# Optimization experiments

Hardware: AMD Instinct MI355X
Metric: run time of the kernel (lower is better)

The kernel has to match this reference:

```python
import jax, jax.numpy as jnp
import numpy as np

D_MODEL = 1024
NUM_HEADS = 8
D_K = D_MODEL // NUM_HEADS


def setup_inputs() -> dict:
    key = jax.random.key(0)
    ks = jax.random.split(key, 11)
    B, S, D = 2, 2048, D_MODEL
    scale = 1.0 / np.sqrt(D)
    return {
        "Q": jax.random.normal(ks[0], (B, S, D), jnp.float32),
        "K": jax.random.normal(ks[1], (B, S, D), jnp.float32),
        "V": jax.random.normal(ks[2], (B, S, D), jnp.float32),
        # torch nn.Linear weights are stored (out_features, in_features)
        "Wq": jax.random.normal(ks[3], (D, D), jnp.float32) * scale,
        "bq": jnp.zeros((D,), jnp.float32),
        "Wk": jax.random.normal(ks[4], (D, D), jnp.float32) * scale,
        "bk": jnp.zeros((D,), jnp.float32),
        "Wv": jax.random.normal(ks[5], (D, D), jnp.float32) * scale,
        "bv": jnp.zeros((D,), jnp.float32),
        "Wo": jax.random.normal(ks[6], (D, D), jnp.float32) * scale,
        "bo": jnp.zeros((D,), jnp.float32),
    }


def reference(Q, K, V, Wq, bq, Wk, bk, Wv, bv, Wo, bo):
    B, S, D = Q.shape
    H, dk = NUM_HEADS, D_K
    # projections (torch Linear: x @ W.T + b), then split heads -> [B,H,S,dk]
    q = (Q @ Wq.T + bq).reshape(B, S, H, dk).transpose(0, 2, 1, 3)
    k = (K @ Wk.T + bk).reshape(B, S, H, dk).transpose(0, 2, 1, 3)
    v = (V @ Wv.T + bv).reshape(B, S, H, dk).transpose(0, 2, 1, 3)
    scores = jnp.einsum("bhqd,bhkd->bhqk", q, k) / jnp.sqrt(jnp.float32(dk))
    attn = jax.nn.softmax(scores, axis=-1)  # [B,H,S,S]
    ctx = jnp.einsum("bhqk,bhkd->bhqd", attn, v)
    concat = ctx.transpose(0, 2, 1, 3).reshape(B, S, D)
    out = concat @ Wo.T + bo
    return out, attn
```

## Files before the change

### kernel.cpp

```cpp
#include <hip/hip_runtime.h>

#define S_LEN 2048
#define DMODEL 1024
#define NHEADS 8
#define DK 128
#define BATCH 2

typedef _Float16 h16;
typedef __attribute__((ext_vector_type(8))) _Float16 half8v;
typedef __attribute__((ext_vector_type(4))) float float4v;

#define GLD16(gp, lp)                                                  \
  __builtin_amdgcn_global_load_lds(                                    \
      (const __attribute__((address_space(1))) void*)(gp),             \
      (__attribute__((address_space(3))) void*)(lp), 16, 0, 0)

__global__ __launch_bounds__(256) void cvt_all(
    const float* __restrict__ q, const float* __restrict__ k, const float* __restrict__ v,
    const float* __restrict__ wq, const float* __restrict__ wk, const float* __restrict__ wv,
    const float* __restrict__ wo,
    h16* __restrict__ dq, h16* __restrict__ dk, h16* __restrict__ dv,
    h16* __restrict__ dwq, h16* __restrict__ dwk, h16* __restrict__ dwv,
    h16* __restrict__ dwo) {
  int i = blockIdx.x * 256 + threadIdx.x;
  const float* src;
  h16* dst;
  int off;
  if (i < 1572864) {
    int seg = i >> 19;
    off = i & 524287;
    src = seg == 0 ? q : (seg == 1 ? k : v);
    dst = seg == 0 ? dq : (seg == 1 ? dk : dv);
  } else {
    int j = i - 1572864;
    int seg = j >> 17;
    off = j & 131071;
    src = seg == 0 ? wq : (seg == 1 ? wk : (seg == 2 ? wv : wo));
    dst = seg == 0 ? dwq : (seg == 1 ? dwk : (seg == 2 ? dwv : dwo));
  }
  const float4* s = (const float4*)src + (size_t)off * 2;
  float4 a = s[0], b = s[1];
  half8v h = {(h16)a.x, (h16)a.y, (h16)a.z, (h16)a.w,
              (h16)b.x, (h16)b.y, (h16)b.z, (h16)b.w};
  *((half8v*)dst + off) = h;
}

__global__ __launch_bounds__(256) void qkv_gemm(
    const h16* __restrict__ qf, const h16* __restrict__ kf, const h16* __restrict__ vf,
    const h16* __restrict__ wq, const h16* __restrict__ wk, const h16* __restrict__ wv,
    const float* __restrict__ bq, const float* __restrict__ bk, const float* __restrict__ bv,
    h16* __restrict__ qh, h16* __restrict__ kh, h16* __restrict__ vt) {
  __shared__ h16 As[128 * 32];
  __shared__ h16 Bs[128 * 32];

  const int z = blockIdx.z;
  const h16* A = z == 0 ? qf : (z == 1 ? kf : vf);
  const h16* Bw = z == 0 ? wq : (z == 1 ? wk : wv);
  const float* bias = z == 0 ? bq : (z == 1 ? bk : bv);
  h16* outp = z == 0 ? qh : (z == 1 ? kh : vt);

  const int t = threadIdx.x, lane = t & 63, w = t >> 6;
  const int m0 = blockIdx.y * 128, n0 = blockIdx.x * 128;
  const int wm = (w >> 1) * 64, wn = (w & 1) * 64;
  const int lcol = lane & 15, lquad = lane >> 4;

  float4v acc[4][4];
  for (int i = 0; i < 4; ++i)
    for (int j = 0; j < 4; ++j) acc[i][j] = {0.f, 0.f, 0.f, 0.f};

  for (int kt = 0; kt < 1024; kt += 32) {
    __syncthreads();
    for (int j = 0; j < 2; ++j) {
      int i = w * 2 + j;
      int row = i * 16 + (lane >> 2);
      int c4 = (lane & 3) ^ ((row >> 1) & 3);
      GLD16(A + (size_t)(m0 + row) * 1024 + kt + c4 * 8, As + i * 512);
      GLD16(Bw + (size_t)(n0 + row) * 1024 + kt + c4 * 8, Bs + i * 512);
    }
    __syncthreads();

    half8v af[4], bf[4];
    for (int mi = 0; mi < 4; ++mi) {
      int r = wm + mi * 16 + lcol;
      af[mi] = *(const half8v*)(As + r * 32 + ((lquad ^ ((r >> 1) & 3)) << 3));
    }
    for (int ni = 0; ni < 4; ++ni) {
      int r = wn + ni * 16 + lcol;
      bf[ni] = *(const half8v*)(Bs + r * 32 + ((lquad ^ ((r >> 1) & 3)) << 3));
    }
    for (int mi = 0; mi < 4; ++mi)
      for (int ni = 0; ni < 4; ++ni)
        acc[mi][ni] = __builtin_amdgcn_mfma_f32_16x16x32_f16(af[mi], bf[ni],
                                                             acc[mi][ni], 0, 0, 0);
  }

  for (int ni = 0; ni < 4; ++ni) {
    int gn = n0 + wn + ni * 16 + lcol;
    float bvv = bias[gn];
    int hh = gn >> 7, dv = gn & 127;
    for (int mi = 0; mi < 4; ++mi) {
      int gmb = m0 + wm + mi * 16 + lquad * 4;
      for (int r = 0; r < 4; ++r) {
        int gm = gmb + r;
        float v = acc[mi][ni][r] + bvv;
        int b = gm >> 11, s = gm & 2047;
        if (z < 2)
          outp[((size_t)(b * NHEADS + hh) * S_LEN + s) * DK + dv] = (h16)v;
        else
          outp[((size_t)(b * NHEADS + hh) * DK + dv) * S_LEN + s] = (h16)v;
      }
    }
  }
}

__global__ __launch_bounds__(256) void out_gemm(const h16* __restrict__ A,
                                                const h16* __restrict__ Bw,
                                                const float* __restrict__ bias,
                                                float* __restrict__ C) {
  __shared__ h16 As[64 * 32];
  __shared__ h16 Bs[128 * 32];

  const int t = threadIdx.x, lane = t & 63, w = t >> 6;
  const int m0 = blockIdx.y * 64, n0 = blockIdx.x * 128;
  const int wm = (w >> 1) * 32, wn = (w & 1) * 64;
  const int lcol = lane & 15, lquad = lane >> 4;

  float4v acc[2][4];
  for (int i = 0; i < 2; ++i)
    for (int j = 0; j < 4; ++j) acc[i][j] = {0.f, 0.f, 0.f, 0.f};

  for (int kt = 0; kt < 1024; kt += 32) {
    __syncthreads();
    {
      int i = w;
      int row = i * 16 + (lane >> 2);
      int c4 = (lane & 3) ^ ((row >> 1) & 3);
      GLD16(A + (size_t)(m0 + row) * 1024 + kt + c4 * 8, As + i * 512);
    }
    for (int j = 0; j < 2; ++j) {
      int i = w * 2 + j;
      int row = i * 16 + (lane >> 2);
      int c4 = (lane & 3) ^ ((row >> 1) & 3);
      GLD16(Bw + (size_t)(n0 + row) * 1024 + kt + c4 * 8, Bs + i * 512);
    }
    __syncthreads();

    half8v af[2], bf[4];
    for (int mi = 0; mi < 2; ++mi) {
      int r = wm + mi * 16 + lcol;
      af[mi] = *(const half8v*)(As + r * 32 + ((lquad ^ ((r >> 1) & 3)) << 3));
    }
    for (int ni = 0; ni < 4; ++ni) {
      int r = wn + ni * 16 + lcol;
      bf[ni] = *(const half8v*)(Bs + r * 32 + ((lquad ^ ((r >> 1) & 3)) << 3));
    }
    for (int mi = 0; mi < 2; ++mi)
      for (int ni = 0; ni < 4; ++ni)
        acc[mi][ni] = __builtin_amdgcn_mfma_f32_16x16x32_f16(af[mi], bf[ni],
                                                             acc[mi][ni], 0, 0, 0);
  }

  for (int ni = 0; ni < 4; ++ni) {
    int gn = n0 + wn + ni * 16 + lcol;
    float bvv = bias[gn];
    for (int mi = 0; mi < 2; ++mi) {
      int gmb = m0 + wm + mi * 16 + lquad * 4;
      for (int r = 0; r < 4; ++r)
        C[(size_t)(gmb + r) * 1024 + gn] = acc[mi][ni][r] + bvv;
    }
  }
}

__device__ inline void attn_bid(int& bh, int& q0) {
  int id = blockIdx.y * 32 + blockIdx.x;
  int xcd = id & 7, rank = id >> 3;
  bh = xcd + 8 * (rank >> 5);
  q0 = (rank & 31) * 64;
}

#define PV_STEP(PP, VV)                                                        \
  {                                                                            \
    half8v ap[4][2];                                                           \
    for (int mi = 0; mi < 4; ++mi)                                             \
      for (int k2 = 0; k2 < 2; ++k2)                                           \
        ap[mi][k2] =                                                           \
            *(const half8v*)((PP) + (mi * 16 + lcol) * 72 + k2 * 32 + lquad * 8); \
    for (int nd = 0; nd < 2; ++nd) {                                           \
      int r = w * 32 + nd * 16 + lcol;                                         \
      for (int k2 = 0; k2 < 2; ++k2) {                                         \
        half8v bv = *(const half8v*)((VV) + r * 64 +                           \
                                     (((k2 * 4 + lquad) ^ (r & 7)) << 3));     \
        for (int mi = 0; mi < 4; ++mi)                                         \
          cacc[mi][nd] = __builtin_amdgcn_mfma_f32_16x16x32_f16(               \
              ap[mi][k2], bv, cacc[mi][nd], 0, 0, 0);                          \
      }                                                                        \
    }                                                                          \
  }

__global__ __launch_bounds__(256, 2) void attn_fused(
    const h16* __restrict__ qh, const h16* __restrict__ kh,
    const h16* __restrict__ vt, float* __restrict__ attn,
    h16* __restrict__ ctxb) {
  __shared__ h16 Ks[64 * 128];
  __shared__ h16 Vts[2][128 * 64];
  __shared__ h16 Ps[2][64 * 72];

  const int t = threadIdx.x, lane = t & 63, w = t >> 6;
  const int lcol = lane & 15, lquad = lane >> 4;
  int bh, q0;
  attn_bid(bh, q0);
  const int b = bh >> 3, h = bh & 7;
  const float scale = 0.08838834764831845f;

  for (int j = 0; j < 4; ++j) {
    int i = w * 4 + j;
    int row = i * 4 + (lane >> 4);
    int c4 = (lane & 15) ^ (row & 7);
    GLD16(qh + ((size_t)bh * S_LEN + q0 + row) * DK + c4 * 8, Ks + i * 512);
  }
  __syncthreads();
  half8v aq[4][4];
  for (int mi = 0; mi < 4; ++mi) {
    int r = mi * 16 + lcol;
    for (int ks = 0; ks < 4; ++ks)
      aq[mi][ks] = *(const half8v*)(Ks + r * 128 + (((ks * 4 + lquad) ^ (r & 7)) << 3));
  }

  float ls[4][4];
  for (int mi = 0; mi < 4; ++mi)
    for (int rr = 0; rr < 4; ++rr) ls[mi][rr] = 0.f;

  for (int kt = 0; kt < 32; ++kt) {
    __syncthreads();
    for (int j = 0; j < 4; ++j) {
      int i = w * 4 + j;
      int row = i * 4 + (lane >> 4);
      int c4 = (lane & 15) ^ (row & 7);
      GLD16(kh + ((size_t)bh * S_LEN + kt * 64 + row) * DK + c4 * 8, Ks + i * 512);
    }
    __syncthreads();

    float4v sacc[4];
    for (int mi = 0; mi < 4; ++mi) sacc[mi] = {0.f, 0.f, 0.f, 0.f};
    int r = w * 16 + lcol;
    for (int ks = 0; ks < 4; ++ks) {
      half8v bk = *(const half8v*)(Ks + r * 128 + (((ks * 4 + lquad) ^ (r & 7)) << 3));
      for (int mi = 0; mi < 4; ++mi)
        sacc[mi] = __builtin_amdgcn_mfma_f32_16x16x32_f16(aq[mi][ks], bk, sacc[mi], 0, 0, 0);
    }
    for (int mi = 0; mi < 4; ++mi)
      for (int rr = 0; rr < 4; ++rr) ls[mi][rr] += __expf(sacc[mi][rr] * scale);
  }

  float* red = (float*)Ps[0];
  for (int mi = 0; mi < 4; ++mi)
    for (int rr = 0; rr < 4; ++rr) {
      float vsum = ls[mi][rr];
      for (int off = 1; off < 16; off <<= 1) vsum += __shfl_xor(vsum, off);
      if (lcol == 0) red[w * 64 + mi * 16 + lquad * 4 + rr] = vsum;
    }
  __syncthreads();
  float il[4][4];
  for (int mi = 0; mi < 4; ++mi)
    for (int rr = 0; rr < 4; ++rr) {
      int row = mi * 16 + lquad * 4 + rr;
      il[mi][rr] = 1.f / (red[row] + red[64 + row] + red[128 + row] + red[192 + row]);
    }

  float4v cacc[4][2];
  for (int mi = 0; mi < 4; ++mi)
    for (int nd = 0; nd < 2; ++nd) cacc[mi][nd] = {0.f, 0.f, 0.f, 0.f};

  float* abase = attn + ((size_t)bh * S_LEN + q0 + lquad * 4) * S_LEN + w * 16 + lcol;

  for (int kt = 0; kt < 32; ++kt) {
    int p = kt & 1;
    __syncthreads();
    for (int j = 0; j < 4; ++j) {
      int i = w * 4 + j;
      int row = i * 4 + (lane >> 4);
      int c4 = (lane & 15) ^ (row & 7);
      GLD16(kh + ((size_t)bh * S_LEN + kt * 64 + row) * DK + c4 * 8, Ks + i * 512);
    }
    for (int j = 0; j < 4; ++j) {
      int i = w * 4 + j;
      int row = i * 8 + (lane >> 3);
      int c4 = (lane & 7) ^ (row & 7);
      GLD16(vt + ((size_t)bh * DK + row) * S_LEN + kt * 64 + c4 * 8, Vts[p] + i * 512);
    }
    __syncthreads();

    if (kt > 0) {
      const h16* Psr = Ps[p ^ 1];
      const h16* Vr = Vts[p ^ 1];
      PV_STEP(Psr, Vr);
    }

    float4v sacc[4];
    for (int mi = 0; mi < 4; ++mi) sacc[mi] = {0.f, 0.f, 0.f, 0.f};
    {
      int r = w * 16 + lcol;
      for (int ks = 0; ks < 4; ++ks) {
        half8v bk = *(const half8v*)(Ks + r * 128 + (((ks * 4 + lquad) ^ (r & 7)) << 3));
        for (int mi = 0; mi < 4; ++mi)
          sacc[mi] = __builtin_amdgcn_mfma_f32_16x16x32_f16(aq[mi][ks], bk, sacc[mi], 0, 0, 0);
      }
    }

    h16* Psw = Ps[p] + lquad * 4 * 72 + w * 16 + lcol;
    float* ab = abase + (size_t)kt * 64;
    for (int mi = 0; mi < 4; ++mi)
      for (int rr = 0; rr < 4; ++rr) {
        float pv = __expf(sacc[mi][rr] * scale) * il[mi][rr];
        ab[(size_t)(mi * 16 + rr) * S_LEN] = pv;
        Psw[(mi * 16 + rr) * 72] = (h16)pv;
      }
  }

  __syncthreads();
  {
    const h16* Psr = Ps[1];
    const h16* Vr = Vts[1];
    PV_STEP(Psr, Vr);
  }

  h16* cb = ctxb + ((size_t)b * S_LEN + q0 + lquad * 4) * DMODEL + h * DK + w * 32;
  for (int mi = 0; mi < 4; ++mi)
    for (int nd = 0; nd < 2; ++nd)
      for (int rr = 0; rr < 4; ++rr)
        cb[(size_t)(mi * 16 + rr) * DMODEL + nd * 16 + lcol] = (h16)cacc[mi][nd][rr];
}

extern "C" void kernel_launch(void* const* d_in, const int* in_sizes, int n_in,
                              void* d_out, int out_size, void* d_ws, size_t ws_size,
                              hipStream_t stream) {
  const float* Q  = (const float*)d_in[0];
  const float* K  = (const float*)d_in[1];
  const float* V  = (const float*)d_in[2];
  const float* Wq = (const float*)d_in[3];
  const float* bq = (const float*)d_in[4];
  const float* Wk = (const float*)d_in[5];
  const float* bk = (const float*)d_in[6];
  const float* Wv = (const float*)d_in[7];
  const float* bv = (const float*)d_in[8];
  const float* Wo = (const float*)d_in[9];
  const float* bo = (const float*)d_in[10];

  float* out  = (float*)d_out;
  float* attn = out + (size_t)BATCH * S_LEN * DMODEL;

  const size_t NTOK = (size_t)BATCH * S_LEN * DMODEL;
  const size_t NW = (size_t)DMODEL * DMODEL;
  h16* qf  = (h16*)d_ws;
  h16* kf  = qf + NTOK;
  h16* vf  = kf + NTOK;
  h16* wqh = vf + NTOK;
  h16* wkh = wqh + NW;
  h16* wvh = wkh + NW;
  h16* woh = wvh + NW;
  h16* qh  = woh + NW;
  h16* kh  = qh + NTOK;
  h16* vt  = kh + NTOK;
  h16* ctxb = qf;

  dim3 gb(256);
  cvt_all<<<dim3(8192), gb, 0, stream>>>(Q, K, V, Wq, Wk, Wv, Wo,
                                         qf, kf, vf, wqh, wkh, wvh, woh);
  qkv_gemm<<<dim3(8, 32, 3), gb, 0, stream>>>(qf, kf, vf, wqh, wkh, wvh,
                                              bq, bk, bv, qh, kh, vt);
  attn_fused<<<dim3(32, 16), gb, 0, stream>>>(qh, kh, vt, attn, ctxb);
  out_gemm<<<dim3(8, 64), gb, 0, stream>>>(ctxb, woh, bo, out);
}
```

Baseline: 471.7 us.

## Double-buffer LDS tiles with explicit waitcnt barriers in GEMMs and attention

The QKV and output GEMMs now use ping-pong LDS buffers. The next K-tile is prefetched through global_load_lds while MFMAs run on the current one, and each iteration ends with a single s_waitcnt+s_barrier instead of two __syncthreads. The attention kernel also double-buffers its K tiles in both passes. Its PV product moves into the same iteration as the score computation with a single P buffer, and a partial vmcnt(16) wait is meant to avoid draining the attention-probability stores each step. The gain should come from overlapping memory latency with compute. The cost is more LDS per block, and the hand-written vmcnt counting relies on the ordering of in-flight loads and stores.

```diff
diff --git a/kernel.cpp b/kernel.cpp
--- a/kernel.cpp
+++ b/kernel.cpp
@@ -14,6 +14,22 @@
   __builtin_amdgcn_global_load_lds(                                    \
       (const __attribute__((address_space(1))) void*)(gp),             \
       (__attribute__((address_space(3))) void*)(lp), 16, 0, 0)
+
+#define BAR_VM0()                                                       \
+  do {                                                                  \
+    asm volatile("s_waitcnt vmcnt(0) lgkmcnt(0)\ns_barrier" ::: "memory"); \
+    __builtin_amdgcn_sched_barrier(0);                                  \
+  } while (0)
+#define BAR_VM16()                                                      \
+  do {                                                                  \
+    asm volatile("s_waitcnt vmcnt(16) lgkmcnt(0)\ns_barrier" ::: "memory"); \
+    __builtin_amdgcn_sched_barrier(0);                                  \
+  } while (0)
+#define BAR_LGKM()                                                      \
+  do {                                                                  \
+    asm volatile("s_waitcnt lgkmcnt(0)\ns_barrier" ::: "memory");       \
+    __builtin_amdgcn_sched_barrier(0);                                  \
+  } while (0)
 
 __global__ __launch_bounds__(256) void cvt_all(
     const float* __restrict__ q, const float* __restrict__ k, const float* __restrict__ v,
@@ -50,8 +66,8 @@
     const h16* __restrict__ wq, const h16* __restrict__ wk, const h16* __restrict__ wv,
     const float* __restrict__ bq, const float* __restrict__ bk, const float* __restrict__ bv,
     h16* __restrict__ qh, h16* __restrict__ kh, h16* __restrict__ vt) {
-  __shared__ h16 As[128 * 32];
-  __shared__ h16 Bs[128 * 32];
+  __shared__ h16 As[2][128 * 32];
+  __shared__ h16 Bs[2][128 * 32];
 
   const int z = blockIdx.z;
   const h16* A = z == 0 ? qf : (z == 1 ? kf : vf);
@@ -68,30 +84,38 @@
   for (int i = 0; i < 4; ++i)
     for (int j = 0; j < 4; ++j) acc[i][j] = {0.f, 0.f, 0.f, 0.f};
 
-  for (int kt = 0; kt < 1024; kt += 32) {
-    __syncthreads();
-    for (int j = 0; j < 2; ++j) {
-      int i = w * 2 + j;
-      int row = i * 16 + (lane >> 2);
-      int c4 = (lane & 3) ^ ((row >> 1) & 3);
-      GLD16(A + (size_t)(m0 + row) * 1024 + kt + c4 * 8, As + i * 512);
-      GLD16(Bw + (size_t)(n0 + row) * 1024 + kt + c4 * 8, Bs + i * 512);
-    }
-    __syncthreads();
-
+#define QKV_STAGE(S, P)                                                    \
+  for (int j = 0; j < 2; ++j) {                                            \
+    int i = w * 2 + j;                                                     \
+    int row = i * 16 + (lane >> 2);                                        \
+    int c4 = (lane & 3) ^ ((row >> 1) & 3);                                \
+    GLD16(A + (size_t)(m0 + row) * 1024 + (S) * 32 + c4 * 8, As[P] + i * 512); \
+    GLD16(Bw + (size_t)(n0 + row) * 1024 + (S) * 32 + c4 * 8, Bs[P] + i * 512); \
+  }
+
+  QKV_STAGE(0, 0);
+  BAR_VM0();
+
+  for (int s = 0; s < 32; ++s) {
+    int sn = s + 1 < 32 ? s + 1 : s;
+    QKV_STAGE(sn, (s + 1) & 1);
+
+    const h16* Ar = As[s & 1];
+    const h16* Br = Bs[s & 1];
     half8v af[4], bf[4];
     for (int mi = 0; mi < 4; ++mi) {
       int r = wm + mi * 16 + lcol;
-      af[mi] = *(const half8v*)(As + r * 32 + ((lquad ^ ((r >> 1) & 3)) << 3));
+      af[mi] = *(const half8v*)(Ar + r * 32 + ((lquad ^ ((r >> 1) & 3)) << 3));
     }
     for (int ni = 0; ni < 4; ++ni) {
       int r = wn + ni * 16 + lcol;
-      bf[ni] = *(const half8v*)(Bs + r * 32 + ((lquad ^ ((r >> 1) & 3)) << 3));
+      bf[ni] = *(const half8v*)(Br + r * 32 + ((lquad ^ ((r >> 1) & 3)) << 3));
     }
     for (int mi = 0; mi < 4; ++mi)
       for (int ni = 0; ni < 4; ++ni)
         acc[mi][ni] = __builtin_amdgcn_mfma_f32_16x16x32_f16(af[mi], bf[ni],
                                                              acc[mi][ni], 0, 0, 0);
+    BAR_VM0();
   }
 
   for (int ni = 0; ni < 4; ++ni) {
@@ -103,11 +127,11 @@
       for (int r = 0; r < 4; ++r) {
         int gm = gmb + r;
         float v = acc[mi][ni][r] + bvv;
-        int b = gm >> 11, s = gm & 2047;
+        int b = gm >> 11, sdx = gm & 2047;
         if (z < 2)
-          outp[((size_t)(b * NHEADS + hh) * S_LEN + s) * DK + dv] = (h16)v;
+          outp[((size_t)(b * NHEADS + hh) * S_LEN + sdx) * DK + dv] = (h16)v;
         else
-          outp[((size_t)(b * NHEADS + hh) * DK + dv) * S_LEN + s] = (h16)v;
+          outp[((size_t)(b * NHEADS + hh) * DK + dv) * S_LEN + sdx] = (h16)v;
       }
     }
   }
@@ -117,8 +141,8 @@
                                                 const h16* __restrict__ Bw,
                                                 const float* __restrict__ bias,
                                                 float* __restrict__ C) {
-  __shared__ h16 As[64 * 32];
-  __shared__ h16 Bs[128 * 32];
+  __shared__ h16 As[2][64 * 32];
+  __shared__ h16 Bs[2][128 * 32];
 
   const int t = threadIdx.x, lane = t & 63, w = t >> 6;
   const int m0 = blockIdx.y * 64, n0 = blockIdx.x * 128;
@@ -129,35 +153,42 @@
   for (int i = 0; i < 2; ++i)
     for (int j = 0; j < 4; ++j) acc[i][j] = {0.f, 0.f, 0.f, 0.f};
 
-  for (int kt = 0; kt < 1024; kt += 32) {
-    __syncthreads();
-    {
-      int i = w;
-      int row = i * 16 + (lane >> 2);
-      int c4 = (lane & 3) ^ ((row >> 1) & 3);
-      GLD16(A + (size_t)(m0 + row) * 1024 + kt + c4 * 8, As + i * 512);
-    }
-    for (int j = 0; j < 2; ++j) {
-      int i = w * 2 + j;
-      int row = i * 16 + (lane >> 2);
-      int c4 = (lane & 3) ^ ((row >> 1) & 3);
-      GLD16(Bw + (size_t)(n0 + row) * 1024 + kt + c4 * 8, Bs + i * 512);
-    }
-    __syncthreads();
-
+#define OUT_STAGE(S, P)                                                    \
+  {                                                                        \
+    int row = w * 16 + (lane >> 2);                                        \
+    int c4 = (lane & 3) ^ ((row >> 1) & 3);                                \
+    GLD16(A + (size_t)(m0 + row) * 1024 + (S) * 32 + c4 * 8, As[P] + w * 512); \
+    for (int j = 0; j < 2; ++j) {                                          \
+      int i = w * 2 + j;                                                   \
+      int row2 = i * 16 + (lane >> 2);                                     \
+      int c42 = (lane & 3) ^ ((row2 >> 1) & 3);                            \
+      GLD16(Bw + (size_t)(n0 + row2) * 1024 + (S) * 32 + c42 * 8, Bs[P] + i * 512); \
+    }                                                                      \
+  }
+
+  OUT_STAGE(0, 0);
+  BAR_VM0();
+
+  for (int s = 0; s < 32; ++s) {
+    int sn = s + 1 < 32 ? s + 1 : s;
+    OUT_STAGE(sn, (s + 1) & 1);
+
+    const h16* Ar = As[s & 1];
+    const h16* Br = Bs[s & 1];
     half8v af[2], bf[4];
     for (int mi = 0; mi < 2; ++mi) {
       int r = wm + mi * 16 + lcol;
-      af[mi] = *(const half8v*)(As + r * 32 + ((lquad ^ ((r >> 1) & 3)) << 3));
+      af[mi] = *(const half8v*)(Ar + r * 32 + ((lquad ^ ((r >> 1) & 3)) << 3));
     }
     for (int ni = 0; ni < 4; ++ni) {
       int r = wn + ni * 16 + lcol;
-      bf[ni] = *(const half8v*)(Bs + r * 32 + ((lquad ^ ((r >> 1) & 3)) << 3));
+      bf[ni] = *(const half8v*)(Br + r * 32 + ((lquad ^ ((r >> 1) & 3)) << 3));
     }
     for (int mi = 0; mi < 2; ++mi)
       for (int ni = 0; ni < 4; ++ni)
         acc[mi][ni] = __builtin_amdgcn_mfma_f32_16x16x32_f16(af[mi], bf[ni],
                                                              acc[mi][ni], 0, 0, 0);
+    BAR_VM0();
   }
 
   for (int ni = 0; ni < 4; ++ni) {
@@ -178,32 +209,13 @@
   q0 = (rank & 31) * 64;
 }
 
-#define PV_STEP(PP, VV)                                                        \
-  {                                                                            \
-    half8v ap[4][2];                                                           \
-    for (int mi = 0; mi < 4; ++mi)                                             \
-      for (int k2 = 0; k2 < 2; ++k2)                                           \
-        ap[mi][k2] =                                                           \
-            *(const half8v*)((PP) + (mi * 16 + lcol) * 72 + k2 * 32 + lquad * 8); \
-    for (int nd = 0; nd < 2; ++nd) {                                           \
-      int r = w * 32 + nd * 16 + lcol;                                         \
-      for (int k2 = 0; k2 < 2; ++k2) {                                         \
-        half8v bv = *(const half8v*)((VV) + r * 64 +                           \
-                                     (((k2 * 4 + lquad) ^ (r & 7)) << 3));     \
-        for (int mi = 0; mi < 4; ++mi)                                         \
-          cacc[mi][nd] = __builtin_amdgcn_mfma_f32_16x16x32_f16(               \
-              ap[mi][k2], bv, cacc[mi][nd], 0, 0, 0);                          \
-      }                                                                        \
-    }                                                                          \
-  }
-
 __global__ __launch_bounds__(256, 2) void attn_fused(
     const h16* __restrict__ qh, const h16* __restrict__ kh,
     const h16* __restrict__ vt, float* __restrict__ attn,
     h16* __restrict__ ctxb) {
-  __shared__ h16 Ks[64 * 128];
+  __shared__ h16 Ks[2][64 * 128];
   __shared__ h16 Vts[2][128 * 64];
-  __shared__ h16 Ps[2][64 * 72];
+  __shared__ h16 Ps[64 * 72];
 
   const int t = threadIdx.x, lane = t & 63, w = t >> 6;
   const int lcol = lane & 15, lquad = lane >> 4;
@@ -212,47 +224,62 @@
   const int b = bh >> 3, h = bh & 7;
   const float scale = 0.08838834764831845f;
 
+#define STAGE_K(KT, BUF)                                                     \
+  for (int j = 0; j < 4; ++j) {                                              \
+    int i = w * 4 + j;                                                       \
+    int row = i * 4 + (lane >> 4);                                           \
+    int c4 = (lane & 15) ^ (row & 7);                                        \
+    GLD16(kh + ((size_t)bh * S_LEN + (KT) * 64 + row) * DK + c4 * 8,         \
+          (BUF) + i * 512);                                                  \
+  }
+#define STAGE_V(KT, BUF)                                                     \
+  for (int j = 0; j < 4; ++j) {                                              \
+    int i = w * 4 + j;                                                       \
+    int row = i * 8 + (lane >> 3);                                           \
+    int c4 = (lane & 7) ^ (row & 7);                                         \
+    GLD16(vt + ((size_t)bh * DK + row) * S_LEN + (KT) * 64 + c4 * 8,         \
+          (BUF) + i * 512);                                                  \
+  }
+
   for (int j = 0; j < 4; ++j) {
     int i = w * 4 + j;
     int row = i * 4 + (lane >> 4);
     int c4 = (lane & 15) ^ (row & 7);
-    GLD16(qh + ((size_t)bh * S_LEN + q0 + row) * DK + c4 * 8, Ks + i * 512);
-  }
-  __syncthreads();
+    GLD16(qh + ((size_t)bh * S_LEN + q0 + row) * DK + c4 * 8, Ks[0] + i * 512);
+  }
+  BAR_VM0();
+  STAGE_K(0, Ks[1]);
   half8v aq[4][4];
   for (int mi = 0; mi < 4; ++mi) {
     int r = mi * 16 + lcol;
     for (int ks = 0; ks < 4; ++ks)
-      aq[mi][ks] = *(const half8v*)(Ks + r * 128 + (((ks * 4 + lquad) ^ (r & 7)) << 3));
-  }
+      aq[mi][ks] = *(const half8v*)(Ks[0] + r * 128 + (((ks * 4 + lquad) ^ (r & 7)) << 3));
+  }
+  BAR_VM0();
 
   float ls[4][4];
   for (int mi = 0; mi < 4; ++mi)
     for (int rr = 0; rr < 4; ++rr) ls[mi][rr] = 0.f;
 
-  for (int kt = 0; kt < 32; ++kt) {
-    __syncthreads();
-    for (int j = 0; j < 4; ++j) {
-      int i = w * 4 + j;
-      int row = i * 4 + (lane >> 4);
-      int c4 = (lane & 15) ^ (row & 7);
-      GLD16(kh + ((size_t)bh * S_LEN + kt * 64 + row) * DK + c4 * 8, Ks + i * 512);
-    }
-    __syncthreads();
-
+  for (int s = 0; s < 32; ++s) {
+    int sn = s + 1 < 32 ? s + 1 : s;
+    STAGE_K(sn, Ks[s & 1]);
+
+    const h16* Kr = Ks[(s + 1) & 1];
     float4v sacc[4];
     for (int mi = 0; mi < 4; ++mi) sacc[mi] = {0.f, 0.f, 0.f, 0.f};
     int r = w * 16 + lcol;
     for (int ks = 0; ks < 4; ++ks) {
-      half8v bk = *(const half8v*)(Ks + r * 128 + (((ks * 4 + lquad) ^ (r & 7)) << 3));
+      half8v bk = *(const half8v*)(Kr + r * 128 + (((ks * 4 + lquad) ^ (r & 7)) << 3));
       for (int mi = 0; mi < 4; ++mi)
         sacc[mi] = __builtin_amdgcn_mfma_f32_16x16x32_f16(aq[mi][ks], bk, sacc[mi], 0, 0, 0);
     }
     for (int mi = 0; mi < 4; ++mi)
       for (int rr = 0; rr < 4; ++rr) ls[mi][rr] += __expf(sacc[mi][rr] * scale);
-  }
-
-  float* red = (float*)Ps[0];
+    BAR_VM0();
+  }
+
+  float* red = (float*)Ps;
   for (int mi = 0; mi < 4; ++mi)
     for (int rr = 0; rr < 4; ++rr) {
       float vsum = ls[mi][rr];
@@ -273,55 +300,57 @@
 
   float* abase = attn + ((size_t)bh * S_LEN + q0 + lquad * 4) * S_LEN + w * 16 + lcol;
 
-  for (int kt = 0; kt < 32; ++kt) {
-    int p = kt & 1;
-    __syncthreads();
-    for (int j = 0; j < 4; ++j) {
-      int i = w * 4 + j;
-      int row = i * 4 + (lane >> 4);
-      int c4 = (lane & 15) ^ (row & 7);
-      GLD16(kh + ((size_t)bh * S_LEN + kt * 64 + row) * DK + c4 * 8, Ks + i * 512);
-    }
-    for (int j = 0; j < 4; ++j) {
-      int i = w * 4 + j;
-      int row = i * 8 + (lane >> 3);
-      int c4 = (lane & 7) ^ (row & 7);
-      GLD16(vt + ((size_t)bh * DK + row) * S_LEN + kt * 64 + c4 * 8, Vts[p] + i * 512);
-    }
-    __syncthreads();
-
-    if (kt > 0) {
-      const h16* Psr = Ps[p ^ 1];
-      const h16* Vr = Vts[p ^ 1];
-      PV_STEP(Psr, Vr);
-    }
-
+  STAGE_K(0, Ks[0]);
+  STAGE_V(0, Vts[0]);
+  BAR_VM0();
+
+  for (int s = 0; s < 32; ++s) {
+    int p = s & 1;
+    int sn = s + 1 < 32 ? s + 1 : s;
+    STAGE_K(sn, Ks[p ^ 1]);
+    STAGE_V(sn, Vts[p ^ 1]);
+
+    const h16* Kr = Ks[p];
     float4v sacc[4];
     for (int mi = 0; mi < 4; ++mi) sacc[mi] = {0.f, 0.f, 0.f, 0.f};
     {
       int r = w * 16 + lcol;
       for (int ks = 0; ks < 4; ++ks) {
-        half8v bk = *(const half8v*)(Ks + r * 128 + (((ks * 4 + lquad) ^ (r & 7)) << 3));
+        half8v bk = *(const half8v*)(Kr + r * 128 + (((ks * 4 + lquad) ^ (r & 7)) << 3));
         for (int mi = 0; mi < 4; ++mi)
           sacc[mi] = __builtin_amdgcn_mfma_f32_16x16x32_f16(aq[mi][ks], bk, sacc[mi], 0, 0, 0);
       }
     }
 
-    h16* Psw = Ps[p] + lquad * 4 * 72 + w * 16 + lcol;
-    float* ab = abase + (size_t)kt * 64;
+    h16* Psw = Ps + lquad * 4 * 72 + w * 16 + lcol;
+    float* ab = abase + (size_t)s * 64;
     for (int mi = 0; mi < 4; ++mi)
       for (int rr = 0; rr < 4; ++rr) {
         float pv = __expf(sacc[mi][rr] * scale) * il[mi][rr];
         ab[(size_t)(mi * 16 + rr) * S_LEN] = pv;
         Psw[(mi * 16 + rr) * 72] = (h16)pv;
       }
-  }
-
-  __syncthreads();
-  {
-    const h16* Psr = Ps[1];
-    const h16* Vr = Vts[1];
-    PV_STEP(Psr, Vr);
+
+    BAR_LGKM();
+
+    {
+      const h16* Vr = Vts[p];
+      half8v ap[4][2];
+      for (int mi = 0; mi < 4; ++mi)
+        for (int k2 = 0; k2 < 2; ++k2)
+          ap[mi][k2] = *(const half8v*)(Ps + (mi * 16 + lcol) * 72 + k2 * 32 + lquad * 8);
+      for (int nd = 0; nd < 2; ++nd) {
+        int r = w * 32 + nd * 16 + lcol;
+        for (int k2 = 0; k2 < 2; ++k2) {
+          half8v bv = *(const half8v*)(Vr + r * 64 + (((k2 * 4 + lquad) ^ (r & 7)) << 3));
+          for (int mi = 0; mi < 4; ++mi)
+            cacc[mi][nd] = __builtin_amdgcn_mfma_f32_16x16x32_f16(ap[mi][k2], bv,
+                                                                  cacc[mi][nd], 0, 0, 0);
+        }
+      }
+    }
+
+    BAR_VM16();
   }
 
   h16* cb = ctxb + ((size_t)b * S_LEN + q0 + lquad * 4) * DMODEL + h * DK + w * 32;
```

New measurement: 478.8 us. About the same (+1.5%).
